# Optimization experiments

Hardware: AMD Instinct MI355X
Metric: run time of the kernel (lower is better)

## Reference

```python
import jax, jax.numpy as jnp
import numpy as np

K = 3  # hardcoded kNN size in the module

def setup_inputs() -> dict:
    key = jax.random.key(0)
    ks = jax.random.split(key, 8)
    B, M, N, C, NC, OUT = 2, 4096, 8192, 512, 20, 512
    def rn(k, sh, sc=1.0):
        return jax.random.normal(k, sh, dtype=jnp.float32) * sc
    return {
        "src_points": rn(ks[0], (B, M, 3)),
        "tgt_points": rn(ks[1], (B, N, 3)),
        "src_features": rn(ks[2], (B, M, C)),
        # semantic_head: Linear(C,128) -> ReLU -> Linear(128,NC)
        "w_sem1": rn(ks[3], (C, 128), 0.04), "b_sem1": jnp.zeros((128,), jnp.float32),
        "w_sem2": rn(ks[4], (128, NC), 0.08), "b_sem2": jnp.zeros((NC,), jnp.float32),
        # upsample_net: Linear(C+NC,256) -> ReLU -> Linear(256,OUT)
        "w_up1": rn(ks[5], (C + NC, 256), 0.04), "b_up1": jnp.zeros((256,), jnp.float32),
        "w_up2": rn(ks[6], (256, OUT), 0.06), "b_up2": jnp.zeros((OUT,), jnp.float32),
    }

def reference(src_points, tgt_points, src_features,
              w_sem1, b_sem1, w_sem2, b_sem2,
              w_up1, b_up1, w_up2, b_up2):
    # semantic logits per source point: [B, M, NC]
    semantic_logits = jax.nn.relu(src_features @ w_sem1 + b_sem1) @ w_sem2 + b_sem2
    # pairwise euclidean distances tgt->src: [B, N, M]
    d2 = (jnp.sum(tgt_points * tgt_points, -1)[:, :, None]
          + jnp.sum(src_points * src_points, -1)[:, None, :]
          - 2.0 * jnp.einsum('bnd,bmd->bnm', tgt_points, src_points))
    dists = jnp.sqrt(jnp.maximum(d2, 0.0))
    # k smallest distances and their indices
    neg_vals, knn_idx = jax.lax.top_k(-dists, K)   # [B, N, K]
    knn_d = -neg_vals                               # gathered distances, [B, N, K]
    # gather neighbor features / semantics: [B, N, K, C] and [B, N, K, NC]
    knn_features = jax.vmap(lambda f, i: f[i])(src_features, knn_idx)
    knn_semantic = jax.vmap(lambda f, i: f[i])(semantic_logits, knn_idx)
    # inverse-distance softmax weights over the K neighbors
    weights = jax.nn.softmax(-knn_d, axis=-1)                       # [B, N, K]
    semantic_weights = jax.nn.softmax(knn_semantic, axis=-1).mean(axis=2)  # [B, N, NC]
    fused_features = jnp.einsum('bnkd,bnk->bnd', knn_features, weights)    # [B, N, C]
    combined = jnp.concatenate([fused_features, semantic_weights], axis=-1)
    upsampled = jax.nn.relu(combined @ w_up1 + b_up1) @ w_up2 + b_up2      # [B, N, OUT]
    return (upsampled, semantic_logits)
```

## Files before the change

kernel.cpp:

```cpp
#include <hip/hip_runtime.h>
#include <math.h>

#define BB 2
#define MM 4096
#define NN 8192
#define CC 512
#define NC 20
#define OUTD 512
#define H1 128
#define H2 256
#define CIN 532
#define KNN 3
#define SPLIT 32
#define CHUNK (MM / SPLIT)
#define CLEN (CHUNK / 4)

#define RR 32
#define HS 264
#define KT2 8
#define KT1 17

#define RO 16
#define FS 520
#define HS2 136
#define TS 512
#define SKT1 16
#define SKT2 4

#define NPREP 544
#define NKNNB (BB * NN / 256 * SPLIT)

typedef __attribute__((ext_vector_type(8))) short s8;
typedef __attribute__((ext_vector_type(4))) float f4;

__device__ inline unsigned short f2bf(float x) {
    unsigned u = __float_as_uint(x);
    unsigned r = (u + 0x7FFFu + ((u >> 16) & 1u)) >> 16;
    return (unsigned short)r;
}
__device__ inline float bf2fs(short u) {
    return __uint_as_float(((unsigned)(unsigned short)u) << 16);
}

__global__ __launch_bounds__(256) void pk_kernel(
    const float* __restrict__ wu1, const float* __restrict__ wu2,
    const float* __restrict__ ws1, const float* __restrict__ ws2,
    unsigned short* __restrict__ w1p, unsigned short* __restrict__ w2p,
    unsigned short* __restrict__ ws1p, unsigned short* __restrict__ ws2p,
    const float* __restrict__ srcp, const float* __restrict__ tgtp,
    float* __restrict__ pd2, unsigned short* __restrict__ pidx)
{
    __shared__ float4 pts[CHUNK];
    const int tid = threadIdx.x;
    const int bx = blockIdx.x;

    if (bx < NPREP) {
        int i = bx * 256 + tid;
        if (i < KT1 * H2 * 32) {
            int kk = i & 31, n = (i >> 5) & 255, kb = i >> 13;
            int k = kb * 32 + kk;
            w1p[i] = f2bf((k < CIN) ? wu1[(size_t)k * H2 + n] : 0.0f);
        }
        if (i < KT2 * OUTD * 32) {
            int kk = i & 31, n = (i >> 5) & 511, kb = i >> 14;
            int k = kb * 32 + kk;
            w2p[i] = f2bf(wu2[(size_t)k * OUTD + n]);
        }
        if (i < SKT1 * H1 * 32) {
            int kk = i & 31, n = (i >> 5) & 127, kb = i >> 12;
            int k = kb * 32 + kk;
            ws1p[i] = f2bf(ws1[(size_t)k * H1 + n]);
        }
        if (i < SKT2 * 32 * 32) {
            int kk = i & 31, n = (i >> 5) & 31, kb = i >> 10;
            int k = kb * 32 + kk;
            ws2p[i] = f2bf((n < NC) ? ws2[(size_t)k * NC + n] : 0.0f);
        }
        return;
    }

    const int bx2 = bx - NPREP;
    const int g = bx2 & 63;
    const int chunk = bx2 >> 6;
    const int t = g * 256 + tid;
    const int bu = g >> 5;
    const int mbase = chunk * CHUNK;

    if (tid < CHUNK) {
        const float* spg = srcp + ((size_t)bu * MM + mbase) * 3;
        float x = spg[tid * 3 + 0];
        float y = spg[tid * 3 + 1];
        float z = spg[tid * 3 + 2];
        pts[tid] = make_float4(x, y, z, x * x + y * y + z * z);
    }
    __syncthreads();

    const float tx = tgtp[(size_t)t * 3 + 0];
    const float ty = tgtp[(size_t)t * 3 + 1];
    const float tz = tgtp[(size_t)t * 3 + 2];
    const float m2x = -2.0f * tx, m2y = -2.0f * ty, m2z = -2.0f * tz;

    float b0[4], b1[4], b2[4];
    int i0[4], i1[4], i2[4];
#pragma unroll
    for (int k = 0; k < 4; ++k) {
        b0[k] = b1[k] = b2[k] = 1e30f;
        i0[k] = i1[k] = i2[k] = 0;
    }

#pragma unroll 4
    for (int m = 0; m < CLEN; ++m) {
#pragma unroll
        for (int k = 0; k < 4; ++k) {
            float4 p = pts[k * CLEN + m];
            float d = fmaf(m2x, p.x, fmaf(m2y, p.y, fmaf(m2z, p.z, p.w)));
            int mi = mbase + k * CLEN + m;
            bool l2 = d < b2[k], l1 = d < b1[k], l0 = d < b0[k];
            b2[k] = l1 ? b1[k] : (l2 ? d : b2[k]); i2[k] = l1 ? i1[k] : (l2 ? mi : i2[k]);
            b1[k] = l0 ? b0[k] : (l1 ? d : b1[k]); i1[k] = l0 ? i0[k] : (l1 ? mi : i1[k]);
            b0[k] = l0 ? d : b0[k];                i0[k] = l0 ? mi : i0[k];
        }
    }
#pragma unroll
    for (int k = 1; k < 4; ++k) {
#pragma unroll
        for (int j = 0; j < 3; ++j) {
            float d = (j == 0) ? b0[k] : (j == 1) ? b1[k] : b2[k];
            int   i = (j == 0) ? i0[k] : (j == 1) ? i1[k] : i2[k];
            bool e2 = d < b2[0], e1 = d < b1[0], e0 = d < b0[0];
            b2[0] = e1 ? b1[0] : (e2 ? d : b2[0]); i2[0] = e1 ? i1[0] : (e2 ? i : i2[0]);
            b1[0] = e0 ? b0[0] : (e1 ? d : b1[0]); i1[0] = e0 ? i0[0] : (e1 ? i : i1[0]);
            b0[0] = e0 ? d : b0[0];                i0[0] = e0 ? i : i0[0];
        }
    }
    size_t o = ((size_t)t * SPLIT + chunk) * KNN;
    pd2[o + 0] = b0[0]; pd2[o + 1] = b1[0]; pd2[o + 2] = b2[0];
    pidx[o + 0] = (unsigned short)i0[0];
    pidx[o + 1] = (unsigned short)i1[0];
    pidx[o + 2] = (unsigned short)i2[0];
}

__global__ __launch_bounds__(256) void sem_kernel(
    const float* __restrict__ feat,
    const unsigned short* __restrict__ ws1p, const unsigned short* __restrict__ ws2p,
    const unsigned short* __restrict__ w1p,
    const float* __restrict__ b1s, const float* __restrict__ b2s,
    float* __restrict__ logits_out, unsigned short* __restrict__ T)
{
    __shared__ __align__(16) char smem[24128];
    unsigned short* sfeat = (unsigned short*)smem;
    unsigned short* Tst   = (unsigned short*)smem;
    unsigned short* shid  = (unsigned short*)(smem + 16640);
    float*          slg   = (float*)(smem + 20992);
    unsigned short* pP    = (unsigned short*)(smem + 23104);
    const int tid = threadIdx.x;
    const int row0 = blockIdx.x * RO;
    const int lane = tid & 63;
    const int wv = tid >> 6;
    const int l15 = lane & 15;
    const int quad = lane >> 4;

    {
        const int r = tid >> 4, p = tid & 15;
        const float4* fr = (const float4*)(feat + (size_t)(row0 + r) * CC);
#pragma unroll
        for (int j = 0; j < 8; ++j) {
            int c4 = j * 16 + p;
            float4 a = fr[c4];
            ushort4 s;
            s.x = f2bf(a.x); s.y = f2bf(a.y); s.z = f2bf(a.z); s.w = f2bf(a.w);
            *(ushort4*)&sfeat[r * FS + c4 * 4] = s;
        }
    }
    __syncthreads();

    f4 asem[2], ah[4];
    {
#pragma unroll
        for (int c = 0; c < 2; ++c) asem[c] = (f4){0.f, 0.f, 0.f, 0.f};
#pragma unroll
        for (int c = 0; c < 4; ++c) ah[c] = (f4){0.f, 0.f, 0.f, 0.f};
        for (int kb = 0; kb < SKT1; ++kb) {
            s8 a = *(const s8*)&sfeat[l15 * FS + kb * 32 + quad * 8];
#pragma unroll
            for (int c = 0; c < 2; ++c) {
                s8 b = *(const s8*)&ws1p[((size_t)(kb * H1 + wv * 32 + c * 16 + l15)) * 32 + quad * 8];
                asem[c] = __builtin_amdgcn_mfma_f32_16x16x32_bf16(a, b, asem[c], 0, 0, 0);
            }
#pragma unroll
            for (int c = 0; c < 4; ++c) {
                s8 b = *(const s8*)&w1p[((size_t)(kb * H2 + wv * 64 + c * 16 + l15)) * 32 + quad * 8];
                ah[c] = __builtin_amdgcn_mfma_f32_16x16x32_bf16(a, b, ah[c], 0, 0, 0);
            }
        }
    }
    __syncthreads();
    {
#pragma unroll
        for (int c = 0; c < 2; ++c) {
            int col = wv * 32 + c * 16 + l15;
            float bias = b1s[col];
#pragma unroll
            for (int i = 0; i < 4; ++i) {
                int rr = quad * 4 + i;
                shid[rr * HS2 + col] = f2bf(fmaxf(asem[c][i] + bias, 0.0f));
            }
        }
#pragma unroll
        for (int c = 0; c < 4; ++c) {
            int col = wv * 64 + c * 16 + l15;
#pragma unroll
            for (int i = 0; i < 4; ++i) {
                int rr = quad * 4 + i;
                Tst[rr * TS + col] = f2bf(ah[c][i]);
            }
        }
    }
    __syncthreads();

    if (wv < 2) {
        f4 acc = (f4){0.f, 0.f, 0.f, 0.f};
        for (int kb = 0; kb < SKT2; ++kb) {
            s8 a = *(const s8*)&shid[l15 * HS2 + kb * 32 + quad * 8];
            s8 b = *(const s8*)&ws2p[((size_t)(kb * 32 + wv * 16 + l15)) * 32 + quad * 8];
            acc = __builtin_amdgcn_mfma_f32_16x16x32_bf16(a, b, acc, 0, 0, 0);
        }
        int col = wv * 16 + l15;
        float bias = (col < NC) ? b2s[col] : 0.0f;
#pragma unroll
        for (int i = 0; i < 4; ++i) {
            int rr = quad * 4 + i;
            float v = acc[i] + bias;
            slg[rr * 33 + col] = v;
            if (col < NC)
                logits_out[(size_t)(row0 + rr) * NC + col] = v;
        }
    }
    __syncthreads();

    if (tid < RO) {
        int r = tid;
        float mx = -1e30f;
        for (int nc = 0; nc < NC; ++nc) mx = fmaxf(mx, slg[r * 33 + nc]);
        float s = 0.0f;
        float e[NC];
#pragma unroll
        for (int nc = 0; nc < NC; ++nc) { e[nc] = __expf(slg[r * 33 + nc] - mx); s += e[nc]; }
        float inv = 1.0f / s;
#pragma unroll
        for (int nc = 0; nc < 32; ++nc)
            pP[r * 32 + nc] = (nc < NC) ? f2bf(e[nc] * inv) : 0;
    }
    __syncthreads();

    {
        s8 a = *(const s8*)&pP[l15 * 32 + quad * 8];
#pragma unroll
        for (int c = 0; c < 4; ++c) {
            s8 b = *(const s8*)&w1p[((size_t)(16 * H2 + wv * 64 + c * 16 + l15)) * 32 + quad * 8];
            f4 acc = (f4){0.f, 0.f, 0.f, 0.f};
            acc = __builtin_amdgcn_mfma_f32_16x16x32_bf16(a, b, acc, 0, 0, 0);
            int col = wv * 64 + c * 16 + l15;
#pragma unroll
            for (int i = 0; i < 4; ++i) {
                int rr = quad * 4 + i;
                Tst[rr * TS + 256 + col] = f2bf(acc[i]);
            }
        }
    }
    __syncthreads();

    {
#pragma unroll
        for (int v = 0; v < 4; ++v) {
            int e = (tid + v * 256) * 8;
            int r = e >> 9, c = e & (TS - 1);
            s8 d = *(const s8*)&Tst[e];
            *(s8*)&T[((size_t)(row0 + r)) * TS + c] = d;
        }
    }
}

__global__ __launch_bounds__(256) void up_kernel(
    const unsigned short* __restrict__ T,
    const float* __restrict__ pd2, const unsigned short* __restrict__ pidx,
    const float* __restrict__ tgtp,
    const unsigned short* __restrict__ w2p,
    const float* __restrict__ b1g, const float* __restrict__ b2g,
    float* __restrict__ out)
{
    __shared__ unsigned short hid[RR * HS];
    __shared__ float sg[RR][3];
    __shared__ int   sj[RR][3];
    __shared__ float pb[RR][4][3];
    __shared__ int   pi[RR][4][3];
    const int tid = threadIdx.x;
    const int row0 = blockIdx.x * RR;
    const int lane = tid & 63;
    const int wv = tid >> 6;
    const int l15 = lane & 15;
    const int quad = lane >> 4;

    if (tid < RR * 4) {
        const int r = tid >> 2, p = tid & 3;
        int row = row0 + r;
        float b0 = 1e30f, b1 = 1e30f, b2 = 1e30f;
        int i0 = 0, i1 = 0, i2 = 0;
        size_t base = (size_t)row * SPLIT * KNN + (size_t)p * 8 * KNN;
#pragma unroll
        for (int j = 0; j < 8 * KNN; ++j) {
            float d = pd2[base + j];
            int m = pidx[base + j];
            bool l2 = d < b2, l1 = d < b1, l0 = d < b0;
            b2 = l1 ? b1 : (l2 ? d : b2); i2 = l1 ? i1 : (l2 ? m : i2);
            b1 = l0 ? b0 : (l1 ? d : b1); i1 = l0 ? i0 : (l1 ? m : i1);
            b0 = l0 ? d : b0;             i0 = l0 ? m : i0;
        }
        pb[r][p][0] = b0; pb[r][p][1] = b1; pb[r][p][2] = b2;
        pi[r][p][0] = i0; pi[r][p][1] = i1; pi[r][p][2] = i2;
    }
    __syncthreads();

    if (tid < RR) {
        int row = row0 + tid;
        float b0 = 1e30f, b1 = 1e30f, b2 = 1e30f;
        int i0 = 0, i1 = 0, i2 = 0;
#pragma unroll
        for (int p = 0; p < 4; ++p)
#pragma unroll
            for (int j = 0; j < 3; ++j) {
                float d = pb[tid][p][j];
                int m = pi[tid][p][j];
                bool l2 = d < b2, l1 = d < b1, l0 = d < b0;
                b2 = l1 ? b1 : (l2 ? d : b2); i2 = l1 ? i1 : (l2 ? m : i2);
                b1 = l0 ? b0 : (l1 ? d : b1); i1 = l0 ? i0 : (l1 ? m : i1);
                b0 = l0 ? d : b0;             i0 = l0 ? m : i0;
            }
        float tx = tgtp[(size_t)row * 3 + 0];
        float ty = tgtp[(size_t)row * 3 + 1];
        float tz = tgtp[(size_t)row * 3 + 2];
        float t2 = tx * tx + ty * ty + tz * tz;
        float d0 = sqrtf(fmaxf(b0 + t2, 0.0f));
        float d1 = sqrtf(fmaxf(b1 + t2, 0.0f));
        float d2v = sqrtf(fmaxf(b2 + t2, 0.0f));
        float e1 = __expf(d0 - d1);
        float e2 = __expf(d0 - d2v);
        float inv = 1.0f / (1.0f + e1 + e2);
        sg[tid][0] = inv; sg[tid][1] = e1 * inv; sg[tid][2] = e2 * inv;
        sj[tid][0] = i0; sj[tid][1] = i1; sj[tid][2] = i2;
    }
    __syncthreads();

    {
        const int r = tid >> 3, p = tid & 7, c0 = p * 32;
        int row = row0 + r;
        size_t bofs = (size_t)(row >> 13) * MM;
        float pre[32];
#pragma unroll
        for (int cc = 0; cc < 32; ++cc) pre[cc] = 0.0f;
#pragma unroll
        for (int k = 0; k < 3; ++k) {
            const unsigned short* Tr = T + (bofs + (size_t)sj[r][k]) * TS;
            float gk = sg[r][k];
#pragma unroll
            for (int v = 0; v < 4; ++v) {
                s8 h = *(const s8*)&Tr[c0 + v * 8];
                s8 g = *(const s8*)&Tr[256 + c0 + v * 8];
#pragma unroll
                for (int e = 0; e < 8; ++e) {
                    pre[v * 8 + e] = fmaf(gk, bf2fs(h[e]), pre[v * 8 + e]);
                    pre[v * 8 + e] = fmaf(1.0f / 3.0f, bf2fs(g[e]), pre[v * 8 + e]);
                }
            }
        }
#pragma unroll
        for (int cc = 0; cc < 32; ++cc) {
            int c = c0 + cc;
            hid[r * HS + c] = f2bf(fmaxf(pre[cc] + b1g[c], 0.0f));
        }
    }
    __syncthreads();

    {
        const int m0 = wv * 128;
        f4 acc2[2][8];
#pragma unroll
        for (int rt = 0; rt < 2; ++rt)
#pragma unroll
            for (int c = 0; c < 8; ++c) acc2[rt][c] = (f4){0.f, 0.f, 0.f, 0.f};
        for (int kb = 0; kb < KT2; ++kb) {
            s8 a0 = *(const s8*)&hid[l15 * HS + kb * 32 + quad * 8];
            s8 a1 = *(const s8*)&hid[(l15 + 16) * HS + kb * 32 + quad * 8];
            s8 bfr[8];
#pragma unroll
            for (int c = 0; c < 8; ++c)
                bfr[c] = *(const s8*)&w2p[((size_t)(kb * OUTD + m0 + c * 16 + l15)) * 32 + quad * 8];
#pragma unroll
            for (int c = 0; c < 8; ++c) {
                acc2[0][c] = __builtin_amdgcn_mfma_f32_16x16x32_bf16(a0, bfr[c], acc2[0][c], 0, 0, 0);
                acc2[1][c] = __builtin_amdgcn_mfma_f32_16x16x32_bf16(a1, bfr[c], acc2[1][c], 0, 0, 0);
            }
        }
#pragma unroll
        for (int c = 0; c < 8; ++c) {
            int ccol = m0 + c * 16 + l15;
            float bias = b2g[ccol];
#pragma unroll
            for (int rt = 0; rt < 2; ++rt)
#pragma unroll
                for (int i = 0; i < 4; ++i) {
                    int rr = rt * 16 + quad * 4 + i;
                    out[(size_t)(row0 + rr) * OUTD + ccol] = acc2[rt][c][i] + bias;
                }
        }
    }
}

extern "C" void kernel_launch(void* const* d_in, const int* in_sizes, int n_in,
                              void* d_out, int out_size, void* d_ws, size_t ws_size,
                              hipStream_t stream) {
    (void)in_sizes; (void)n_in; (void)out_size; (void)ws_size;
    const float* src_points   = (const float*)d_in[0];
    const float* tgt_points   = (const float*)d_in[1];
    const float* src_features = (const float*)d_in[2];
    const float* w_sem1 = (const float*)d_in[3];
    const float* b_sem1 = (const float*)d_in[4];
    const float* w_sem2 = (const float*)d_in[5];
    const float* b_sem2 = (const float*)d_in[6];
    const float* w_up1  = (const float*)d_in[7];
    const float* b_up1  = (const float*)d_in[8];
    const float* w_up2  = (const float*)d_in[9];
    const float* b_up2  = (const float*)d_in[10];

    float* out    = (float*)d_out;
    float* ups    = out;
    float* logits = out + (size_t)BB * NN * OUTD;

    char* w = (char*)d_ws;
    unsigned short* T = (unsigned short*)w;    w += (size_t)BB * MM * TS * 2;
    float* pd2  = (float*)w;                   w += (size_t)BB * NN * SPLIT * KNN * 4;
    unsigned short* pidx = (unsigned short*)w; w += (size_t)BB * NN * SPLIT * KNN * 2;
    unsigned short* w1p  = (unsigned short*)w; w += (size_t)KT1 * H2 * 32 * 2;
    unsigned short* w2p  = (unsigned short*)w; w += (size_t)KT2 * OUTD * 32 * 2;
    unsigned short* ws1p = (unsigned short*)w; w += (size_t)SKT1 * H1 * 32 * 2;
    unsigned short* ws2p = (unsigned short*)w; w += (size_t)SKT2 * 32 * 32 * 2;

    pk_kernel<<<dim3(NPREP + NKNNB), dim3(256), 0, stream>>>(
        w_up1, w_up2, w_sem1, w_sem2, w1p, w2p, ws1p, ws2p,
        src_points, tgt_points, pd2, pidx);
    sem_kernel<<<dim3(BB * MM / RO), dim3(256), 0, stream>>>(
        src_features, ws1p, ws2p, w1p, b_sem1, b_sem2, logits, T);
    up_kernel<<<dim3(BB * NN / RR), dim3(256), 0, stream>>>(
        T, pd2, pidx, tgt_points, w2p, b_up1, b_up2, ups);
}
```

Before: 165.1 us.

## Split weight prep into own kernel and fuse kNN with semantic head launch

Weight packing now runs in a small standalone kernel. The kNN partial search and the semantic-head/T computation are merged into one launch, with block-index ranges choosing the role. The aim is to let the ALU-bound kNN blocks and the MFMA-bound semantic blocks share the GPU at the same time, and to remove a serialization point between the two kernels. In exchange, the fused kernel carries the larger register and shared-memory footprint of both paths, which can lower occupancy for the kNN blocks.

```diff
diff --git a/kernel.cpp b/kernel.cpp
--- a/kernel.cpp
+++ b/kernel.cpp
@@ -29,6 +29,7 @@
 
 #define NPREP 544
 #define NKNNB (BB * NN / 256 * SPLIT)
+#define NSEMB (BB * MM / RO)
 
 typedef __attribute__((ext_vector_type(8))) short s8;
 typedef __attribute__((ext_vector_type(4))) float f4;
@@ -42,105 +43,38 @@
     return __uint_as_float(((unsigned)(unsigned short)u) << 16);
 }
 
-__global__ __launch_bounds__(256) void pk_kernel(
+__global__ __launch_bounds__(256) void prep_kernel(
     const float* __restrict__ wu1, const float* __restrict__ wu2,
     const float* __restrict__ ws1, const float* __restrict__ ws2,
     unsigned short* __restrict__ w1p, unsigned short* __restrict__ w2p,
-    unsigned short* __restrict__ ws1p, unsigned short* __restrict__ ws2p,
+    unsigned short* __restrict__ ws1p, unsigned short* __restrict__ ws2p)
+{
+    int i = blockIdx.x * 256 + threadIdx.x;
+    if (i < KT1 * H2 * 32) {
+        int kk = i & 31, n = (i >> 5) & 255, kb = i >> 13;
+        int k = kb * 32 + kk;
+        w1p[i] = f2bf((k < CIN) ? wu1[(size_t)k * H2 + n] : 0.0f);
+    }
+    if (i < KT2 * OUTD * 32) {
+        int kk = i & 31, n = (i >> 5) & 511, kb = i >> 14;
+        int k = kb * 32 + kk;
+        w2p[i] = f2bf(wu2[(size_t)k * OUTD + n]);
+    }
+    if (i < SKT1 * H1 * 32) {
+        int kk = i & 31, n = (i >> 5) & 127, kb = i >> 12;
+        int k = kb * 32 + kk;
+        ws1p[i] = f2bf(ws1[(size_t)k * H1 + n]);
+    }
+    if (i < SKT2 * 32 * 32) {
+        int kk = i & 31, n = (i >> 5) & 31, kb = i >> 10;
+        int k = kb * 32 + kk;
+        ws2p[i] = f2bf((n < NC) ? ws2[(size_t)k * NC + n] : 0.0f);
+    }
+}
+
+__global__ __launch_bounds__(256) void fused_kernel(
     const float* __restrict__ srcp, const float* __restrict__ tgtp,
-    float* __restrict__ pd2, unsigned short* __restrict__ pidx)
-{
-    __shared__ float4 pts[CHUNK];
-    const int tid = threadIdx.x;
-    const int bx = blockIdx.x;
-
-    if (bx < NPREP) {
-        int i = bx * 256 + tid;
-        if (i < KT1 * H2 * 32) {
-            int kk = i & 31, n = (i >> 5) & 255, kb = i >> 13;
-            int k = kb * 32 + kk;
-            w1p[i] = f2bf((k < CIN) ? wu1[(size_t)k * H2 + n] : 0.0f);
-        }
-        if (i < KT2 * OUTD * 32) {
-            int kk = i & 31, n = (i >> 5) & 511, kb = i >> 14;
-            int k = kb * 32 + kk;
-            w2p[i] = f2bf(wu2[(size_t)k * OUTD + n]);
-        }
-        if (i < SKT1 * H1 * 32) {
-            int kk = i & 31, n = (i >> 5) & 127, kb = i >> 12;
-            int k = kb * 32 + kk;
-            ws1p[i] = f2bf(ws1[(size_t)k * H1 + n]);
-        }
-        if (i < SKT2 * 32 * 32) {
-            int kk = i & 31, n = (i >> 5) & 31, kb = i >> 10;
-            int k = kb * 32 + kk;
-            ws2p[i] = f2bf((n < NC) ? ws2[(size_t)k * NC + n] : 0.0f);
-        }
-        return;
-    }
-
-    const int bx2 = bx - NPREP;
-    const int g = bx2 & 63;
-    const int chunk = bx2 >> 6;
-    const int t = g * 256 + tid;
-    const int bu = g >> 5;
-    const int mbase = chunk * CHUNK;
-
-    if (tid < CHUNK) {
-        const float* spg = srcp + ((size_t)bu * MM + mbase) * 3;
-        float x = spg[tid * 3 + 0];
-        float y = spg[tid * 3 + 1];
-        float z = spg[tid * 3 + 2];
-        pts[tid] = make_float4(x, y, z, x * x + y * y + z * z);
-    }
-    __syncthreads();
-
-    const float tx = tgtp[(size_t)t * 3 + 0];
-    const float ty = tgtp[(size_t)t * 3 + 1];
-    const float tz = tgtp[(size_t)t * 3 + 2];
-    const float m2x = -2.0f * tx, m2y = -2.0f * ty, m2z = -2.0f * tz;
-
-    float b0[4], b1[4], b2[4];
-    int i0[4], i1[4], i2[4];
-#pragma unroll
-    for (int k = 0; k < 4; ++k) {
-        b0[k] = b1[k] = b2[k] = 1e30f;
-        i0[k] = i1[k] = i2[k] = 0;
-    }
-
-#pragma unroll 4
-    for (int m = 0; m < CLEN; ++m) {
-#pragma unroll
-        for (int k = 0; k < 4; ++k) {
-            float4 p = pts[k * CLEN + m];
-            float d = fmaf(m2x, p.x, fmaf(m2y, p.y, fmaf(m2z, p.z, p.w)));
-            int mi = mbase + k * CLEN + m;
-            bool l2 = d < b2[k], l1 = d < b1[k], l0 = d < b0[k];
-            b2[k] = l1 ? b1[k] : (l2 ? d : b2[k]); i2[k] = l1 ? i1[k] : (l2 ? mi : i2[k]);
-            b1[k] = l0 ? b0[k] : (l1 ? d : b1[k]); i1[k] = l0 ? i0[k] : (l1 ? mi : i1[k]);
-            b0[k] = l0 ? d : b0[k];                i0[k] = l0 ? mi : i0[k];
-        }
-    }
-#pragma unroll
-    for (int k = 1; k < 4; ++k) {
-#pragma unroll
-        for (int j = 0; j < 3; ++j) {
-            float d = (j == 0) ? b0[k] : (j == 1) ? b1[k] : b2[k];
-            int   i = (j == 0) ? i0[k] : (j == 1) ? i1[k] : i2[k];
-            bool e2 = d < b2[0], e1 = d < b1[0], e0 = d < b0[0];
-            b2[0] = e1 ? b1[0] : (e2 ? d : b2[0]); i2[0] = e1 ? i1[0] : (e2 ? i : i2[0]);
-            b1[0] = e0 ? b0[0] : (e1 ? d : b1[0]); i1[0] = e0 ? i0[0] : (e1 ? i : i1[0]);
-            b0[0] = e0 ? d : b0[0];                i0[0] = e0 ? i : i0[0];
-        }
-    }
-    size_t o = ((size_t)t * SPLIT + chunk) * KNN;
-    pd2[o + 0] = b0[0]; pd2[o + 1] = b1[0]; pd2[o + 2] = b2[0];
-    pidx[o + 0] = (unsigned short)i0[0];
-    pidx[o + 1] = (unsigned short)i1[0];
-    pidx[o + 2] = (unsigned short)i2[0];
-}
-
-__global__ __launch_bounds__(256) void sem_kernel(
+    float* __restrict__ pd2, unsigned short* __restrict__ pidx,
     const float* __restrict__ feat,
     const unsigned short* __restrict__ ws1p, const unsigned short* __restrict__ ws2p,
     const unsigned short* __restrict__ w1p,
@@ -148,13 +82,78 @@
     float* __restrict__ logits_out, unsigned short* __restrict__ T)
 {
     __shared__ __align__(16) char smem[24128];
+    const int tid = threadIdx.x;
+    const int bx = blockIdx.x;
+
+    if (bx < NKNNB) {
+        float4* pts = (float4*)smem;
+        const int g = bx & 63;
+        const int chunk = bx >> 6;
+        const int t = g * 256 + tid;
+        const int bu = g >> 5;
+        const int mbase = chunk * CHUNK;
+
+        if (tid < CHUNK) {
+            const float* spg = srcp + ((size_t)bu * MM + mbase) * 3;
+            float x = spg[tid * 3 + 0];
+            float y = spg[tid * 3 + 1];
+            float z = spg[tid * 3 + 2];
+            pts[tid] = make_float4(x, y, z, x * x + y * y + z * z);
+        }
+        __syncthreads();
+
+        const float tx = tgtp[(size_t)t * 3 + 0];
+        const float ty = tgtp[(size_t)t * 3 + 1];
+        const float tz = tgtp[(size_t)t * 3 + 2];
+        const float m2x = -2.0f * tx, m2y = -2.0f * ty, m2z = -2.0f * tz;
+
+        float b0[4], b1[4], b2[4];
+        int i0[4], i1[4], i2[4];
+#pragma unroll
+        for (int k = 0; k < 4; ++k) {
+            b0[k] = b1[k] = b2[k] = 1e30f;
+            i0[k] = i1[k] = i2[k] = 0;
+        }
+
+#pragma unroll 4
+        for (int m = 0; m < CLEN; ++m) {
+#pragma unroll
+            for (int k = 0; k < 4; ++k) {
+                float4 p = pts[k * CLEN + m];
+                float d = fmaf(m2x, p.x, fmaf(m2y, p.y, fmaf(m2z, p.z, p.w)));
+                int mi = mbase + k * CLEN + m;
+                bool l2 = d < b2[k], l1 = d < b1[k], l0 = d < b0[k];
+                b2[k] = l1 ? b1[k] : (l2 ? d : b2[k]); i2[k] = l1 ? i1[k] : (l2 ? mi : i2[k]);
+                b1[k] = l0 ? b0[k] : (l1 ? d : b1[k]); i1[k] = l0 ? i0[k] : (l1 ? mi : i1[k]);
+                b0[k] = l0 ? d : b0[k];                i0[k] = l0 ? mi : i0[k];
+            }
+        }
+#pragma unroll
+        for (int k = 1; k < 4; ++k) {
+#pragma unroll
+            for (int j = 0; j < 3; ++j) {
+                float d = (j == 0) ? b0[k] : (j == 1) ? b1[k] : b2[k];
+                int   i = (j == 0) ? i0[k] : (j == 1) ? i1[k] : i2[k];
+                bool e2 = d < b2[0], e1 = d < b1[0], e0 = d < b0[0];
+                b2[0] = e1 ? b1[0] : (e2 ? d : b2[0]); i2[0] = e1 ? i1[0] : (e2 ? i : i2[0]);
+                b1[0] = e0 ? b0[0] : (e1 ? d : b1[0]); i1[0] = e0 ? i0[0] : (e1 ? i : i1[0]);
+                b0[0] = e0 ? d : b0[0];                i0[0] = e0 ? i : i0[0];
+            }
+        }
+        size_t o = ((size_t)t * SPLIT + chunk) * KNN;
+        pd2[o + 0] = b0[0]; pd2[o + 1] = b1[0]; pd2[o + 2] = b2[0];
+        pidx[o + 0] = (unsigned short)i0[0];
+        pidx[o + 1] = (unsigned short)i1[0];
+        pidx[o + 2] = (unsigned short)i2[0];
+        return;
+    }
+
     unsigned short* sfeat = (unsigned short*)smem;
     unsigned short* Tst   = (unsigned short*)smem;
     unsigned short* shid  = (unsigned short*)(smem + 16640);
     float*          slg   = (float*)(smem + 20992);
     unsigned short* pP    = (unsigned short*)(smem + 23104);
-    const int tid = threadIdx.x;
-    const int row0 = blockIdx.x * RO;
+    const int row0 = (bx - NKNNB) * RO;
     const int lane = tid & 63;
     const int wv = tid >> 6;
     const int l15 = lane & 15;
@@ -445,10 +444,10 @@
     unsigned short* ws1p = (unsigned short*)w; w += (size_t)SKT1 * H1 * 32 * 2;
     unsigned short* ws2p = (unsigned short*)w; w += (size_t)SKT2 * 32 * 32 * 2;
 
-    pk_kernel<<<dim3(NPREP + NKNNB), dim3(256), 0, stream>>>(
-        w_up1, w_up2, w_sem1, w_sem2, w1p, w2p, ws1p, ws2p,
-        src_points, tgt_points, pd2, pidx);
-    sem_kernel<<<dim3(BB * MM / RO), dim3(256), 0, stream>>>(
+    prep_kernel<<<dim3(NPREP), dim3(256), 0, stream>>>(
+        w_up1, w_up2, w_sem1, w_sem2, w1p, w2p, ws1p, ws2p);
+    fused_kernel<<<dim3(NKNNB + NSEMB), dim3(256), 0, stream>>>(
+        src_points, tgt_points, pd2, pidx,
         src_features, ws1p, ws2p, w1p, b_sem1, b_sem2, logits, T);
     up_kernel<<<dim3(BB * NN / RR), dim3(256), 0, stream>>>(
         T, pd2, pidx, tgt_points, w2p, b_up1, b_up2, ups);
```

New measurement: 159.0 us. 3.7% less time.
